# Kernel tuning notes

Hardware: AMD Instinct MI355X
Metric: run time of the kernel (lower is better)

## Reference

```python
import jax, jax.numpy as jnp
import numpy as np

HEADS = 12

def setup_inputs() -> dict:
    key = jax.random.key(0)
    ks = jax.random.split(key, 6)
    dim = 768
    x  = jax.random.normal(ks[0], (2, 4096, dim), dtype=jnp.float32)
    s = dim ** -0.5
    wq = jax.random.normal(ks[1], (dim, dim), dtype=jnp.float32) * s
    wk = jax.random.normal(ks[2], (dim, dim), dtype=jnp.float32) * s
    wv = jax.random.normal(ks[3], (dim, dim), dtype=jnp.float32) * s
    wo = jax.random.normal(ks[4], (dim, dim), dtype=jnp.float32) * s
    bo = jnp.zeros((dim,), dtype=jnp.float32)
    return {"x": x, "wq": wq, "wk": wk, "wv": wv, "wo": wo, "bo": bo}

def reference(x, wq, wk, wv, wo, bo):
    b, n, dim = x.shape
    h = HEADS
    d = dim // h
    scale = d ** -0.5
    # nn.Linear(dim, dim, bias=False): y = x @ W.T ; weights stored [out, in]
    def proj(w):
        return (x @ w.T).reshape(b, n, h, d).transpose(0, 2, 1, 3)  # b h n d
    q, k, v = proj(wq), proj(wk), proj(wv)
    dots = jnp.einsum('bhqd,bhkd->bhqk', q, k) * scale  # full N x N scores
    attn = jax.nn.softmax(dots, axis=-1)
    out = jnp.einsum('bhqk,bhkd->bhqd', attn, v)
    out = out.transpose(0, 2, 1, 3).reshape(b, n, dim)
    # to_out: Linear(dim, dim) + Dropout (identity at inference)
    return out @ wo.T + bo
```

## Files before the change

kernel.cpp:

```cpp
#include <hip/hip_runtime.h>
#include <hip/hip_bf16.h>


#define HEADS 12
#define NSEQ  4096
#define DIM   768
#define DH    64
#define BATCH 2
#define QSCALE 0.18033688f

typedef __attribute__((ext_vector_type(8))) short bf16x8;
typedef __attribute__((ext_vector_type(4))) float f32x4;
typedef __attribute__((ext_vector_type(4))) short bf16x4;

static __device__ __forceinline__ short f2bf(float f) {
    __hip_bfloat16 h = __float2bfloat16(f);
    return *reinterpret_cast<short*>(&h);
}

static __device__ __forceinline__ unsigned pkbf(float a, float b) {
    unsigned ua = __float_as_uint(a), ub = __float_as_uint(b);
    ua += 0x7FFFu + ((ua >> 16) & 1u);
    ub += 0x7FFFu + ((ub >> 16) & 1u);
    return __builtin_amdgcn_perm(ub, ua, 0x07060302);
}

#define GLL(g, l) __builtin_amdgcn_global_load_lds( \
    (const __attribute__((address_space(1))) void*)(g), \
    (__attribute__((address_space(3))) void*)(l), 16, 0, 0)

#define NX (BATCH*NSEQ*DIM)
#define NW (DIM*DIM)

__global__ __launch_bounds__(256) void convert_kernel(
    const float* __restrict__ x,  const float* __restrict__ wq,
    const float* __restrict__ wk, const float* __restrict__ wv,
    const float* __restrict__ wo,
    short* __restrict__ xb, short* __restrict__ wqb, short* __restrict__ wkb,
    short* __restrict__ wvb, short* __restrict__ wob)
{
    int i = (blockIdx.x * 256 + threadIdx.x) * 4;
    const float* src; short* dst; int off;
    if      (i < NX)          { src = x;  dst = xb;  off = i; }
    else if (i < NX + NW)     { src = wq; dst = wqb; off = i - NX; }
    else if (i < NX + 2*NW)   { src = wk; dst = wkb; off = i - NX - NW; }
    else if (i < NX + 3*NW)   { src = wv; dst = wvb; off = i - NX - 2*NW; }
    else                      { src = wo; dst = wob; off = i - NX - 3*NW; }
    float4 f = *(const float4*)(src + off);
    bf16x4 o; o[0] = f2bf(f.x); o[1] = f2bf(f.y); o[2] = f2bf(f.z); o[3] = f2bf(f.w);
    *(bf16x4*)(dst + off) = o;
}

__global__ __launch_bounds__(256, 4) void qkv_proj_kernel(
    const short* __restrict__ xb, const short* __restrict__ wqb,
    const short* __restrict__ wkb, const short* __restrict__ wvb,
    short* __restrict__ qb, short* __restrict__ kb, short* __restrict__ vtb)
{
    __shared__ __align__(16) short As[2][128*32];
    __shared__ __align__(16) short Bs[2][128*32];

    const int wave = threadIdx.x >> 6, lane = threadIdx.x & 63;
    const int lr = lane & 15, lq = lane >> 4;
    const int which = blockIdx.y / 6;
    const short* __restrict__ W = (which == 0) ? wqb : ((which == 1) ? wkb : wvb);
    const int m0  = blockIdx.x * 128;
    const int o0l = (blockIdx.y % 6) * 128;

    const short* __restrict__ gA = xb + (size_t)(m0  + wave*32 + (lane>>2)) * DIM + (lane&3)*8;
    const short* __restrict__ gB = W  + (size_t)(o0l + wave*32 + (lane>>2)) * DIM + (lane&3)*8;

    const int wm = (wave & 1) * 64, wn = (wave >> 1) * 64;

    f32x4 acc[4][4];
    #pragma unroll
    for (int i = 0; i < 4; i++)
        #pragma unroll
        for (int j = 0; j < 4; j++) acc[i][j] = (f32x4){0.f, 0.f, 0.f, 0.f};

    GLL(gA,            &As[0][(wave*32     )*32]);
    GLL(gA + 16*DIM,   &As[0][(wave*32 + 16)*32]);
    GLL(gB,            &Bs[0][(wave*32     )*32]);
    GLL(gB + 16*DIM,   &Bs[0][(wave*32 + 16)*32]);
    __syncthreads();

    for (int kt = 0; kt < 24; kt++) {
        const int p = kt & 1;
        if (kt < 23) {
            const int k1 = (kt + 1) * 32;
            GLL(gA + k1,          &As[1-p][(wave*32     )*32]);
            GLL(gA + k1 + 16*DIM, &As[1-p][(wave*32 + 16)*32]);
            GLL(gB + k1,          &Bs[1-p][(wave*32     )*32]);
            GLL(gB + k1 + 16*DIM, &Bs[1-p][(wave*32 + 16)*32]);
        }
        bf16x8 a[4], b[4];
        #pragma unroll
        for (int i = 0; i < 4; i++)
            a[i] = *(const bf16x8*)&As[p][(wm + i*16 + lr)*32 + lq*8];
        #pragma unroll
        for (int j = 0; j < 4; j++)
            b[j] = *(const bf16x8*)&Bs[p][(wn + j*16 + lr)*32 + lq*8];
        #pragma unroll
        for (int i = 0; i < 4; i++)
            #pragma unroll
            for (int j = 0; j < 4; j++)
                acc[i][j] = __builtin_amdgcn_mfma_f32_16x16x32_bf16(a[i], b[j], acc[i][j], 0, 0, 0);
        __syncthreads();
    }

    if (which == 2) {
        #pragma unroll
        for (int i = 0; i < 4; i++)
            #pragma unroll
            for (int j = 0; j < 4; j++) {
                const int mb = m0 + wm + i*16 + lq*4;
                const int o  = o0l + wn + j*16 + lr;
                const int bb = mb >> 12, n0 = mb & (NSEQ - 1);
                const int h  = o >> 6,   dd = o & 63;
                bf16x4 v;
                #pragma unroll
                for (int r = 0; r < 4; r++) v[r] = f2bf(acc[i][j][r]);
                *(bf16x4*)(vtb + ((size_t)(bb*HEADS + h) * DH + dd) * NSEQ + n0) = v;
            }
    } else {
        short* __restrict__ dst = (which == 0) ? qb : kb;
        const float scale = (which == 0) ? QSCALE : 1.0f;
        #pragma unroll
        for (int i = 0; i < 4; i++)
            #pragma unroll
            for (int j = 0; j < 4; j++)
                #pragma unroll
                for (int r = 0; r < 4; r++) {
                    const int m  = m0 + wm + i*16 + lq*4 + r;
                    const int o  = o0l + wn + j*16 + lr;
                    const int bb = m >> 12, n = m & (NSEQ - 1);
                    const int h  = o >> 6,  dd = o & 63;
                    dst[(((size_t)(bb*HEADS + h) * NSEQ) + n) * DH + dd] = f2bf(acc[i][j][r] * scale);
                }
    }
}

__global__ __launch_bounds__(256, 3) void attn_kernel(
    const short* __restrict__ qb, const short* __restrict__ kb,
    const short* __restrict__ vtb, short* __restrict__ ob)
{
    __shared__ __align__(16) short Ks[2][64*64];
    __shared__ __align__(16) short Vs[2][64*64];
    __shared__ __align__(16) short Vones[16*64];
    __shared__ __align__(16) short Ps[4][2][16*64];

    const int wave = threadIdx.x >> 6, lane = threadIdx.x & 63;
    const int lrow = lane & 15, lquad = lane >> 4;

    const int flat = blockIdx.x;
    const int xcd  = flat & 7;
    const int idx  = flat >> 3;
    const int bh   = xcd * 3 + (idx % 3);
    const int qblk = idx / 3;
    const int b = bh / HEADS, h = bh % HEADS;
    const int q0 = qblk * 128 + wave * 32;

    const short* __restrict__ Q  = qb  + (size_t)bh * NSEQ * DH;
    const short* __restrict__ K  = kb  + (size_t)bh * NSEQ * DH;
    const short* __restrict__ Vt = vtb + (size_t)bh * DH * NSEQ;

    for (int i = threadIdx.x; i < 16*64; i += 256) Vones[i] = 0x3F80;

    const int t  = threadIdx.x;
    const int r2 = t >> 3, cc = t & 7;
    const int ccs = (cc ^ (r2 & 7)) * 8;

    bf16x8 aq[2][2];
    #pragma unroll
    for (int rb = 0; rb < 2; rb++)
        #pragma unroll
        for (int kk = 0; kk < 2; kk++)
            aq[rb][kk] = *(const bf16x8*)(Q + (size_t)(q0 + rb*16 + lrow) * DH + kk*32 + lquad*8);

    f32x4 oacc[2][5];
    #pragma unroll
    for (int rb = 0; rb < 2; rb++)
        #pragma unroll
        for (int ct = 0; ct < 5; ct++) oacc[rb][ct] = (f32x4){0.f, 0.f, 0.f, 0.f};

    {
        bf16x8 k0a = *(const bf16x8*)(K  + (size_t)(r2     ) * DH   + cc*8);
        bf16x8 k0b = *(const bf16x8*)(K  + (size_t)(r2 + 32) * DH   + cc*8);
        bf16x8 v0a = *(const bf16x8*)(Vt + (size_t)(r2     ) * NSEQ + cc*8);
        bf16x8 v0b = *(const bf16x8*)(Vt + (size_t)(r2 + 32) * NSEQ + cc*8);
        *(bf16x8*)&Ks[0][ r2     *64 + ccs] = k0a;
        *(bf16x8*)&Ks[0][(r2+32) *64 + ccs] = k0b;
        *(bf16x8*)&Vs[0][ r2     *64 + ccs] = v0a;
        *(bf16x8*)&Vs[0][(r2+32) *64 + ccs] = v0b;
    }
    __syncthreads();

    bf16x8 bv4[2];
    #pragma unroll
    for (int kk = 0; kk < 2; kk++)
        bv4[kk] = *(const bf16x8*)&Vones[lrow*64 + (((kk*4 + lquad) ^ (lrow & 7)) * 8)];

    for (int kt = 0; kt < NSEQ / 64; kt++) {
        const int p = kt & 1;
        bf16x8 kr0, kr1, vr0, vr1;
        if (kt + 1 < NSEQ / 64) {
            const int key1 = (kt + 1) * 64;
            kr0 = *(const bf16x8*)(K  + (size_t)(key1 + r2     ) * DH   + cc*8);
            kr1 = *(const bf16x8*)(K  + (size_t)(key1 + r2 + 32) * DH   + cc*8);
            vr0 = *(const bf16x8*)(Vt + (size_t)(r2     ) * NSEQ + key1 + cc*8);
            vr1 = *(const bf16x8*)(Vt + (size_t)(r2 + 32) * NSEQ + key1 + cc*8);
        }

        bf16x8 ak[4][2];
        #pragma unroll
        for (int ct = 0; ct < 4; ct++)
            #pragma unroll
            for (int kk = 0; kk < 2; kk++)
                ak[ct][kk] = *(const bf16x8*)&Ks[p][(ct*16 + lrow)*64 + (((kk*4 + lquad) ^ (lrow & 7)) * 8)];

        #pragma unroll
        for (int rb = 0; rb < 2; rb++) {
            f32x4 s[4];
            #pragma unroll
            for (int ct = 0; ct < 4; ct++) s[ct] = (f32x4){0.f, 0.f, 0.f, 0.f};
            #pragma unroll
            for (int kk = 0; kk < 2; kk++)
                #pragma unroll
                for (int ct = 0; ct < 4; ct++)
                    s[ct] = __builtin_amdgcn_mfma_f32_16x16x32_bf16(ak[ct][kk], aq[rb][kk], s[ct], 0, 0, 0);
            #pragma unroll
            for (int ct = 0; ct < 4; ct++) {
                const float e0 = __builtin_amdgcn_exp2f(s[ct][0]);
                const float e1 = __builtin_amdgcn_exp2f(s[ct][1]);
                const float e2 = __builtin_amdgcn_exp2f(s[ct][2]);
                const float e3 = __builtin_amdgcn_exp2f(s[ct][3]);
                const unsigned lo = pkbf(e0, e1), hi = pkbf(e2, e3);
                const int cps = (((ct*2 + (lquad >> 1)) ^ (lrow & 7)) * 8) + (lquad & 1) * 4;
                *(uint2*)&Ps[wave][rb][lrow*64 + cps] = (uint2){lo, hi};
            }
        }

        bf16x8 bv[4][2];
        #pragma unroll
        for (int ct = 0; ct < 4; ct++)
            #pragma unroll
            for (int kk = 0; kk < 2; kk++)
                bv[ct][kk] = *(const bf16x8*)&Vs[p][(ct*16 + lrow)*64 + (((kk*4 + lquad) ^ (lrow & 7)) * 8)];

        #pragma unroll
        for (int rb = 0; rb < 2; rb++) {
            bf16x8 ap[2];
            #pragma unroll
            for (int kk = 0; kk < 2; kk++)
                ap[kk] = *(const bf16x8*)&Ps[wave][rb][lrow*64 + (((kk*4 + lquad) ^ (lrow & 7)) * 8)];
            #pragma unroll
            for (int kk = 0; kk < 2; kk++) {
                #pragma unroll
                for (int ct = 0; ct < 4; ct++)
                    oacc[rb][ct] = __builtin_amdgcn_mfma_f32_16x16x32_bf16(ap[kk], bv[ct][kk], oacc[rb][ct], 0, 0, 0);
                oacc[rb][4] = __builtin_amdgcn_mfma_f32_16x16x32_bf16(ap[kk], bv4[kk], oacc[rb][4], 0, 0, 0);
            }
        }

        if (kt + 1 < NSEQ / 64) {
            *(bf16x8*)&Ks[1-p][ r2     *64 + ccs] = kr0;
            *(bf16x8*)&Ks[1-p][(r2+32) *64 + ccs] = kr1;
            *(bf16x8*)&Vs[1-p][ r2     *64 + ccs] = vr0;
            *(bf16x8*)&Vs[1-p][(r2+32) *64 + ccs] = vr1;
        }
        __syncthreads();
    }

    #pragma unroll
    for (int rb = 0; rb < 2; rb++)
        #pragma unroll
        for (int r = 0; r < 4; r++) {
            const float inv = __builtin_amdgcn_rcpf(oacc[rb][4][r]);
            const int n = q0 + rb*16 + lquad*4 + r;
            #pragma unroll
            for (int ct = 0; ct < 4; ct++) {
                const int col = h*DH + ct*16 + lrow;
                ob[((size_t)b * NSEQ + n) * DIM + col] = f2bf(oacc[rb][ct][r] * inv);
            }
        }
}

__global__ __launch_bounds__(256, 4) void out_proj_kernel(
    const short* __restrict__ xo, const short* __restrict__ W,
    const float* __restrict__ bias, float* __restrict__ y)
{
    __shared__ __align__(16) short As[2][128*32];
    __shared__ __align__(16) short Bs[2][128*32];

    const int wave = threadIdx.x >> 6, lane = threadIdx.x & 63;
    const int lr = lane & 15, lq = lane >> 4;
    const int m0 = blockIdx.x * 128;
    const int o0 = blockIdx.y * 128;

    const short* __restrict__ gA = xo + (size_t)(m0 + wave*32 + (lane>>2)) * DIM + (lane&3)*8;
    const short* __restrict__ gB = W  + (size_t)(o0 + wave*32 + (lane>>2)) * DIM + (lane&3)*8;

    const int wm = (wave & 1) * 64, wn = (wave >> 1) * 64;

    f32x4 acc[4][4];
    #pragma unroll
    for (int i = 0; i < 4; i++)
        #pragma unroll
        for (int j = 0; j < 4; j++) acc[i][j] = (f32x4){0.f, 0.f, 0.f, 0.f};

    GLL(gA,            &As[0][(wave*32     )*32]);
    GLL(gA + 16*DIM,   &As[0][(wave*32 + 16)*32]);
    GLL(gB,            &Bs[0][(wave*32     )*32]);
    GLL(gB + 16*DIM,   &Bs[0][(wave*32 + 16)*32]);
    __syncthreads();

    for (int kt = 0; kt < 24; kt++) {
        const int p = kt & 1;
        if (kt < 23) {
            const int k1 = (kt + 1) * 32;
            GLL(gA + k1,          &As[1-p][(wave*32     )*32]);
            GLL(gA + k1 + 16*DIM, &As[1-p][(wave*32 + 16)*32]);
            GLL(gB + k1,          &Bs[1-p][(wave*32     )*32]);
            GLL(gB + k1 + 16*DIM, &Bs[1-p][(wave*32 + 16)*32]);
        }
        bf16x8 a[4], b[4];
        #pragma unroll
        for (int i = 0; i < 4; i++)
            a[i] = *(const bf16x8*)&As[p][(wm + i*16 + lr)*32 + lq*8];
        #pragma unroll
        for (int j = 0; j < 4; j++)
            b[j] = *(const bf16x8*)&Bs[p][(wn + j*16 + lr)*32 + lq*8];
        #pragma unroll
        for (int i = 0; i < 4; i++)
            #pragma unroll
            for (int j = 0; j < 4; j++)
                acc[i][j] = __builtin_amdgcn_mfma_f32_16x16x32_bf16(a[i], b[j], acc[i][j], 0, 0, 0);
        __syncthreads();
    }

    #pragma unroll
    for (int i = 0; i < 4; i++)
        #pragma unroll
        for (int j = 0; j < 4; j++)
            #pragma unroll
            for (int r = 0; r < 4; r++) {
                const int m = m0 + wm + i*16 + lq*4 + r;
                const int o = o0 + wn + j*16 + lr;
                y[(size_t)m * DIM + o] = acc[i][j][r] + bias[o];
            }
}

extern "C" void kernel_launch(void* const* d_in, const int* in_sizes, int n_in,
                              void* d_out, int out_size, void* d_ws, size_t ws_size,
                              hipStream_t stream) {
    const float* x  = (const float*)d_in[0];
    const float* wq = (const float*)d_in[1];
    const float* wk = (const float*)d_in[2];
    const float* wv = (const float*)d_in[3];
    const float* wo = (const float*)d_in[4];
    const float* bo = (const float*)d_in[5];
    float* out = (float*)d_out;

    const size_t qkv_elems = (size_t)BATCH * HEADS * NSEQ * DH;
    short* xb  = (short*)d_ws;
    short* wqb = xb  + NX;
    short* wkb = wqb + NW;
    short* wvb = wkb + NW;
    short* wob = wvb + NW;
    short* qb  = wob + NW;
    short* kb  = qb  + qkv_elems;
    short* vtb = kb  + qkv_elems;
    short* ob  = xb;

    dim3 blk(256);
    convert_kernel <<<dim3((NX + 4*NW) / 1024), blk, 0, stream>>>(x, wq, wk, wv, wo,
                                                                  xb, wqb, wkb, wvb, wob);
    qkv_proj_kernel<<<dim3(64, 18), blk, 0, stream>>>(xb, wqb, wkb, wvb, qb, kb, vtb);
    attn_kernel    <<<dim3(768), blk, 0, stream>>>(qb, kb, vtb, ob);
    out_proj_kernel<<<dim3(64, 6), blk, 0, stream>>>(ob, wob, bo, out);
}
```

Baseline: 280.9 us.

## Give attention waves 64 query rows and vectorize projection epilogue stores

The attention kernel now runs 128-thread blocks of two waves, each handling 64 query rows instead of 32. Each K/V tile loaded into shared memory is therefore reused across more MFMA work per wave, and fewer waves split the same 128-query block. The Q/K projection and output projection swap MFMA operand order so each lane holds 4 consecutive output columns. That lets the epilogues use vector bf16x4 or float4 stores and a float4 bias load instead of scalar stores. The risks are higher register pressure from 4x5 accumulators per wave and fewer waves per block to hide latency.

```diff
diff --git a/kernel.cpp b/kernel.cpp
--- a/kernel.cpp
+++ b/kernel.cpp
@@ -99,11 +99,19 @@
         #pragma unroll
         for (int j = 0; j < 4; j++)
             b[j] = *(const bf16x8*)&Bs[p][(wn + j*16 + lr)*32 + lq*8];
-        #pragma unroll
-        for (int i = 0; i < 4; i++)
-            #pragma unroll
-            for (int j = 0; j < 4; j++)
-                acc[i][j] = __builtin_amdgcn_mfma_f32_16x16x32_bf16(a[i], b[j], acc[i][j], 0, 0, 0);
+        if (which == 2) {
+            #pragma unroll
+            for (int i = 0; i < 4; i++)
+                #pragma unroll
+                for (int j = 0; j < 4; j++)
+                    acc[i][j] = __builtin_amdgcn_mfma_f32_16x16x32_bf16(a[i], b[j], acc[i][j], 0, 0, 0);
+        } else {
+            #pragma unroll
+            for (int i = 0; i < 4; i++)
+                #pragma unroll
+                for (int j = 0; j < 4; j++)
+                    acc[i][j] = __builtin_amdgcn_mfma_f32_16x16x32_bf16(b[j], a[i], acc[i][j], 0, 0, 0);
+        }
         __syncthreads();
     }
 
@@ -127,26 +135,27 @@
         #pragma unroll
         for (int i = 0; i < 4; i++)
             #pragma unroll
-            for (int j = 0; j < 4; j++)
-                #pragma unroll
-                for (int r = 0; r < 4; r++) {
-                    const int m  = m0 + wm + i*16 + lq*4 + r;
-                    const int o  = o0l + wn + j*16 + lr;
-                    const int bb = m >> 12, n = m & (NSEQ - 1);
-                    const int h  = o >> 6,  dd = o & 63;
-                    dst[(((size_t)(bb*HEADS + h) * NSEQ) + n) * DH + dd] = f2bf(acc[i][j][r] * scale);
-                }
-    }
-}
-
-__global__ __launch_bounds__(256, 3) void attn_kernel(
+            for (int j = 0; j < 4; j++) {
+                const int m   = m0 + wm + i*16 + lr;
+                const int ob_ = o0l + wn + j*16 + lq*4;
+                const int bb  = m >> 12, n = m & (NSEQ - 1);
+                const int h   = ob_ >> 6, dd = ob_ & 63;
+                bf16x4 v;
+                #pragma unroll
+                for (int r = 0; r < 4; r++) v[r] = f2bf(acc[i][j][r] * scale);
+                *(bf16x4*)(dst + (((size_t)(bb*HEADS + h) * NSEQ) + n) * DH + dd) = v;
+            }
+    }
+}
+
+__global__ __launch_bounds__(128, 2) void attn_kernel(
     const short* __restrict__ qb, const short* __restrict__ kb,
     const short* __restrict__ vtb, short* __restrict__ ob)
 {
     __shared__ __align__(16) short Ks[2][64*64];
     __shared__ __align__(16) short Vs[2][64*64];
     __shared__ __align__(16) short Vones[16*64];
-    __shared__ __align__(16) short Ps[4][2][16*64];
+    __shared__ __align__(16) short Ps[2][4][16*64];
 
     const int wave = threadIdx.x >> 6, lane = threadIdx.x & 63;
     const int lrow = lane & 15, lquad = lane >> 4;
@@ -157,40 +166,39 @@
     const int bh   = xcd * 3 + (idx % 3);
     const int qblk = idx / 3;
     const int b = bh / HEADS, h = bh % HEADS;
-    const int q0 = qblk * 128 + wave * 32;
+    const int q0 = qblk * 128 + wave * 64;
 
     const short* __restrict__ Q  = qb  + (size_t)bh * NSEQ * DH;
     const short* __restrict__ K  = kb  + (size_t)bh * NSEQ * DH;
     const short* __restrict__ Vt = vtb + (size_t)bh * DH * NSEQ;
 
-    for (int i = threadIdx.x; i < 16*64; i += 256) Vones[i] = 0x3F80;
+    for (int i = threadIdx.x; i < 16*64; i += 128) Vones[i] = 0x3F80;
 
     const int t  = threadIdx.x;
     const int r2 = t >> 3, cc = t & 7;
     const int ccs = (cc ^ (r2 & 7)) * 8;
 
-    bf16x8 aq[2][2];
-    #pragma unroll
-    for (int rb = 0; rb < 2; rb++)
+    bf16x8 aq[4][2];
+    #pragma unroll
+    for (int rb = 0; rb < 4; rb++)
         #pragma unroll
         for (int kk = 0; kk < 2; kk++)
             aq[rb][kk] = *(const bf16x8*)(Q + (size_t)(q0 + rb*16 + lrow) * DH + kk*32 + lquad*8);
 
-    f32x4 oacc[2][5];
-    #pragma unroll
-    for (int rb = 0; rb < 2; rb++)
+    f32x4 oacc[4][5];
+    #pragma unroll
+    for (int rb = 0; rb < 4; rb++)
         #pragma unroll
         for (int ct = 0; ct < 5; ct++) oacc[rb][ct] = (f32x4){0.f, 0.f, 0.f, 0.f};
 
     {
-        bf16x8 k0a = *(const bf16x8*)(K  + (size_t)(r2     ) * DH   + cc*8);
-        bf16x8 k0b = *(const bf16x8*)(K  + (size_t)(r2 + 32) * DH   + cc*8);
-        bf16x8 v0a = *(const bf16x8*)(Vt + (size_t)(r2     ) * NSEQ + cc*8);
-        bf16x8 v0b = *(const bf16x8*)(Vt + (size_t)(r2 + 32) * NSEQ + cc*8);
-        *(bf16x8*)&Ks[0][ r2     *64 + ccs] = k0a;
-        *(bf16x8*)&Ks[0][(r2+32) *64 + ccs] = k0b;
-        *(bf16x8*)&Vs[0][ r2     *64 + ccs] = v0a;
-        *(bf16x8*)&Vs[0][(r2+32) *64 + ccs] = v0b;
+        #pragma unroll
+        for (int rr = 0; rr < 4; rr++) {
+            bf16x8 kv = *(const bf16x8*)(K  + (size_t)(r2 + rr*16) * DH   + cc*8);
+            bf16x8 vv = *(const bf16x8*)(Vt + (size_t)(r2 + rr*16) * NSEQ + cc*8);
+            *(bf16x8*)&Ks[0][(r2 + rr*16)*64 + ccs] = kv;
+            *(bf16x8*)&Vs[0][(r2 + rr*16)*64 + ccs] = vv;
+        }
     }
     __syncthreads();
 
@@ -201,13 +209,14 @@
 
     for (int kt = 0; kt < NSEQ / 64; kt++) {
         const int p = kt & 1;
-        bf16x8 kr0, kr1, vr0, vr1;
+        bf16x8 kr[4], vr[4];
         if (kt + 1 < NSEQ / 64) {
             const int key1 = (kt + 1) * 64;
-            kr0 = *(const bf16x8*)(K  + (size_t)(key1 + r2     ) * DH   + cc*8);
-            kr1 = *(const bf16x8*)(K  + (size_t)(key1 + r2 + 32) * DH   + cc*8);
-            vr0 = *(const bf16x8*)(Vt + (size_t)(r2     ) * NSEQ + key1 + cc*8);
-            vr1 = *(const bf16x8*)(Vt + (size_t)(r2 + 32) * NSEQ + key1 + cc*8);
+            #pragma unroll
+            for (int rr = 0; rr < 4; rr++) {
+                kr[rr] = *(const bf16x8*)(K  + (size_t)(key1 + r2 + rr*16) * DH   + cc*8);
+                vr[rr] = *(const bf16x8*)(Vt + (size_t)(r2 + rr*16) * NSEQ + key1 + cc*8);
+            }
         }
 
         bf16x8 ak[4][2];
@@ -218,7 +227,7 @@
                 ak[ct][kk] = *(const bf16x8*)&Ks[p][(ct*16 + lrow)*64 + (((kk*4 + lquad) ^ (lrow & 7)) * 8)];
 
         #pragma unroll
-        for (int rb = 0; rb < 2; rb++) {
+        for (int rb = 0; rb < 4; rb++) {
             f32x4 s[4];
             #pragma unroll
             for (int ct = 0; ct < 4; ct++) s[ct] = (f32x4){0.f, 0.f, 0.f, 0.f};
@@ -247,7 +256,7 @@
                 bv[ct][kk] = *(const bf16x8*)&Vs[p][(ct*16 + lrow)*64 + (((kk*4 + lquad) ^ (lrow & 7)) * 8)];
 
         #pragma unroll
-        for (int rb = 0; rb < 2; rb++) {
+        for (int rb = 0; rb < 4; rb++) {
             bf16x8 ap[2];
             #pragma unroll
             for (int kk = 0; kk < 2; kk++)
@@ -262,16 +271,17 @@
         }
 
         if (kt + 1 < NSEQ / 64) {
-            *(bf16x8*)&Ks[1-p][ r2     *64 + ccs] = kr0;
-            *(bf16x8*)&Ks[1-p][(r2+32) *64 + ccs] = kr1;
-            *(bf16x8*)&Vs[1-p][ r2     *64 + ccs] = vr0;
-            *(bf16x8*)&Vs[1-p][(r2+32) *64 + ccs] = vr1;
+            #pragma unroll
+            for (int rr = 0; rr < 4; rr++) {
+                *(bf16x8*)&Ks[1-p][(r2 + rr*16)*64 + ccs] = kr[rr];
+                *(bf16x8*)&Vs[1-p][(r2 + rr*16)*64 + ccs] = vr[rr];
+            }
         }
         __syncthreads();
     }
 
     #pragma unroll
-    for (int rb = 0; rb < 2; rb++)
+    for (int rb = 0; rb < 4; rb++)
         #pragma unroll
         for (int r = 0; r < 4; r++) {
             const float inv = __builtin_amdgcn_rcpf(oacc[rb][4][r]);
@@ -333,20 +343,25 @@
         for (int i = 0; i < 4; i++)
             #pragma unroll
             for (int j = 0; j < 4; j++)
-                acc[i][j] = __builtin_amdgcn_mfma_f32_16x16x32_bf16(a[i], b[j], acc[i][j], 0, 0, 0);
+                acc[i][j] = __builtin_amdgcn_mfma_f32_16x16x32_bf16(b[j], a[i], acc[i][j], 0, 0, 0);
         __syncthreads();
     }
 
     #pragma unroll
-    for (int i = 0; i < 4; i++)
-        #pragma unroll
-        for (int j = 0; j < 4; j++)
-            #pragma unroll
-            for (int r = 0; r < 4; r++) {
-                const int m = m0 + wm + i*16 + lq*4 + r;
-                const int o = o0 + wn + j*16 + lr;
-                y[(size_t)m * DIM + o] = acc[i][j][r] + bias[o];
-            }
+    for (int j = 0; j < 4; j++) {
+        const int o = o0 + wn + j*16 + lq*4;
+        const float4 bv = *(const float4*)&bias[o];
+        #pragma unroll
+        for (int i = 0; i < 4; i++) {
+            const int m = m0 + wm + i*16 + lr;
+            float4 v;
+            v.x = acc[i][j][0] + bv.x;
+            v.y = acc[i][j][1] + bv.y;
+            v.z = acc[i][j][2] + bv.z;
+            v.w = acc[i][j][3] + bv.w;
+            *(float4*)&y[(size_t)m * DIM + o] = v;
+        }
+    }
 }
 
 extern "C" void kernel_launch(void* const* d_in, const int* in_sizes, int n_in,
@@ -371,10 +386,9 @@
     short* vtb = kb  + qkv_elems;
     short* ob  = xb;
 
-    dim3 blk(256);
-    convert_kernel <<<dim3((NX + 4*NW) / 1024), blk, 0, stream>>>(x, wq, wk, wv, wo,
-                                                                  xb, wqb, wkb, wvb, wob);
-    qkv_proj_kernel<<<dim3(64, 18), blk, 0, stream>>>(xb, wqb, wkb, wvb, qb, kb, vtb);
-    attn_kernel    <<<dim3(768), blk, 0, stream>>>(qb, kb, vtb, ob);
-    out_proj_kernel<<<dim3(64, 6), blk, 0, stream>>>(ob, wob, bo, out);
-}
+    convert_kernel <<<dim3((NX + 4*NW) / 1024), dim3(256), 0, stream>>>(x, wq, wk, wv, wo,
+                                                                        xb, wqb, wkb, wvb, wob);
+    qkv_proj_kernel<<<dim3(64, 18), dim3(256), 0, stream>>>(xb, wqb, wkb, wvb, qb, kb, vtb);
+    attn_kernel    <<<dim3(768), dim3(128), 0, stream>>>(qb, kb, vtb, ob);
+    out_proj_kernel<<<dim3(64, 6), dim3(256), 0, stream>>>(ob, wob, bo, out);
+}
```

Result: slower. 488.6 us (+74.0%).
